# Optimization experiments

Measured on AMD Instinct MI355X. Metric: run time of the kernel, lower is better.

## Reference

```python
import jax, jax.numpy as jnp
import numpy as np

N = 50000      # nodes
E = 800000     # edges (before self-loops)
IN_DIM = 128
HID = 32
HEADS = 8
OUT_DIM = 16
NEG_SLOPE = 0.2  # PyG GATConv default


def setup_inputs() -> dict:
    key = jax.random.key(0)
    ks = jax.random.split(key, 12)
    x = jax.random.normal(ks[0], (N, IN_DIM), dtype=jnp.float32)
    edge_index = jax.random.randint(ks[1], (2, E), 0, N, dtype=jnp.int32)
    s = 0.1
    # layer 1: GATConv(IN_DIM -> HID, heads=HEADS, concat=True)
    W1 = jax.random.normal(ks[2], (IN_DIM, HEADS * HID), dtype=jnp.float32) * s
    a_src1 = jax.random.normal(ks[3], (HEADS, HID), dtype=jnp.float32) * s
    a_dst1 = jax.random.normal(ks[4], (HEADS, HID), dtype=jnp.float32) * s
    b1 = jax.random.normal(ks[5], (HEADS * HID,), dtype=jnp.float32) * s
    # layer 2: GATConv(HEADS*HID -> HID, heads=1, concat=True)
    W2 = jax.random.normal(ks[6], (HEADS * HID, HID), dtype=jnp.float32) * s
    a_src2 = jax.random.normal(ks[7], (1, HID), dtype=jnp.float32) * s
    a_dst2 = jax.random.normal(ks[8], (1, HID), dtype=jnp.float32) * s
    b2 = jax.random.normal(ks[9], (HID,), dtype=jnp.float32) * s
    # output Linear(HID -> OUT_DIM)
    Wout = jax.random.normal(ks[10], (HID, OUT_DIM), dtype=jnp.float32) * s
    bout = jax.random.normal(ks[11], (OUT_DIM,), dtype=jnp.float32) * s
    return {"x": x, "edge_index": edge_index, "W1": W1, "a_src1": a_src1,
            "a_dst1": a_dst1, "b1": b1, "W2": W2, "a_src2": a_src2,
            "a_dst2": a_dst2, "b2": b2, "Wout": Wout, "bout": bout}


def _gat_conv(x, src, dst, W, a_src, a_dst, b, num_nodes):
    """PyG GATConv (eval mode): linear proj, edge attention logits,
    segment-softmax over incoming edges per dst node, weighted scatter-sum.
    src/dst already include self-loops. Returns [N, H, D]."""
    H, D = a_src.shape
    h = (x @ W).reshape(num_nodes, H, D)                 # [N,H,D]
    alpha_s = jnp.einsum('nhd,hd->nh', h, a_src)         # [N,H]
    alpha_d = jnp.einsum('nhd,hd->nh', h, a_dst)         # [N,H]
    e = jax.nn.leaky_relu(alpha_s[src] + alpha_d[dst], NEG_SLOPE)  # [Etot,H]
    # numerically-stable segment softmax over edges grouped by dst
    m = jax.ops.segment_max(e, dst, num_segments=num_nodes)        # [N,H]
    ex = jnp.exp(e - m[dst])
    den = jax.ops.segment_sum(ex, dst, num_segments=num_nodes)     # [N,H]
    alpha = ex / (den[dst] + 1e-16)                                 # [Etot,H]
    out = jax.ops.segment_sum(alpha[:, :, None] * h[src], dst,
                              num_segments=num_nodes)               # [N,H,D]
    return out, b


def reference(x, edge_index, W1, a_src1, a_dst1, b1, W2, a_src2, a_dst2, b2,
              Wout, bout):
    n = x.shape[0]
    loop = jnp.arange(n, dtype=edge_index.dtype)
    src = jnp.concatenate([edge_index[0], loop])  # PyG add_self_loops=True
    dst = jnp.concatenate([edge_index[1], loop])
    o1, _ = _gat_conv(x, src, dst, W1, a_src1, a_dst1, b1, n)
    h1 = jax.nn.elu(o1.reshape(n, -1) + b1)       # concat heads -> [N, H*D]
    o2, _ = _gat_conv(h1, src, dst, W2, a_src2, a_dst2, b2, n)
    h2 = jax.nn.elu(o2.reshape(n, -1) + b2)       # heads=1 -> [N, HID]
    return h2 @ Wout + bout                        # [N, OUT_DIM]
```

## Files before the change

### kernel.cpp

```cpp
#include <hip/hip_runtime.h>
#include <math.h>

#define IN_DIM 128
#define HID 32
#define HEADS 8
#define OUT_DIM 16
#define NEG_SLOPE 0.2f


__global__ void count_kernel(const int* __restrict__ ei, int* __restrict__ counts,
                             int E, int N) {
    int e = blockIdx.x * 256 + threadIdx.x;
    int Etot = E + N;
    if (e >= Etot) return;
    int dst = (e < E) ? ei[E + e] : (e - E);
    atomicAdd(&counts[dst], 1);
}

__global__ __launch_bounds__(1024) void scan_kernel(const int* __restrict__ counts,
                                                    int* __restrict__ off,
                                                    int* __restrict__ pos, int N) {
    __shared__ int wsum[16];
    __shared__ int wbase[16];
    __shared__ int running_s;
    int tid = threadIdx.x;
    int lane = tid & 63, wid = tid >> 6;
    if (tid == 0) running_s = 0;
    __syncthreads();
    const int CH = 4096;
    int nchunk = (N + CH - 1) / CH;
    for (int c = 0; c < nchunk; ++c) {
        int base_i = c * CH + tid * 4;
        int v0 = (base_i + 0 < N) ? counts[base_i + 0] : 0;
        int v1 = (base_i + 1 < N) ? counts[base_i + 1] : 0;
        int v2 = (base_i + 2 < N) ? counts[base_i + 2] : 0;
        int v3 = (base_i + 3 < N) ? counts[base_i + 3] : 0;
        int tsum = v0 + v1 + v2 + v3;
        int x = tsum;
        #pragma unroll
        for (int ofs = 1; ofs < 64; ofs <<= 1) {
            int y = __shfl_up(x, ofs, 64);
            if (lane >= ofs) x += y;
        }
        if (lane == 63) wsum[wid] = x;
        __syncthreads();
        if (wid == 0) {
            int w = (lane < 16) ? wsum[lane] : 0;
            #pragma unroll
            for (int ofs = 1; ofs < 64; ofs <<= 1) {
                int y = __shfl_up(w, ofs, 64);
                if (lane >= ofs) w += y;
            }
            if (lane < 16) wbase[lane] = w;
        }
        __syncthreads();
        int chunk_base = running_s;
        int wave_excl = (wid == 0) ? 0 : wbase[wid - 1];
        int thr_excl = x - tsum;
        int b = chunk_base + wave_excl + thr_excl;
        if (base_i + 0 < N) { off[base_i + 0] = b; pos[base_i + 0] = b; } b += v0;
        if (base_i + 1 < N) { off[base_i + 1] = b; pos[base_i + 1] = b; } b += v1;
        if (base_i + 2 < N) { off[base_i + 2] = b; pos[base_i + 2] = b; } b += v2;
        if (base_i + 3 < N) { off[base_i + 3] = b; pos[base_i + 3] = b; }
        __syncthreads();
        if (tid == 0) running_s = chunk_base + wbase[15];
        __syncthreads();
    }
    if (tid == 0) off[N] = running_s;
}

__global__ void fill_kernel(const int* __restrict__ ei, int* __restrict__ pos,
                            int* __restrict__ csr_src, int E, int N) {
    int e = blockIdx.x * 256 + threadIdx.x;
    int Etot = E + N;
    if (e >= Etot) return;
    int src, dst;
    if (e < E) { src = ei[e]; dst = ei[E + e]; }
    else       { src = e - E; dst = e - E; }
    int idx = atomicAdd(&pos[dst], 1);
    csr_src[idx] = src;
}

__global__ __launch_bounds__(256) void gemm1_kernel(const float* __restrict__ x,
                                                    const float* __restrict__ W,
                                                    float* __restrict__ hp, int N) {
    __shared__ float4 xs4[32 * 32];
    int n0 = blockIdx.x * 32;
    int t = threadIdx.x;
    int rows = min(32, N - n0);
    const float4* xg = (const float4*)(x + (size_t)n0 * IN_DIM);
    int nf4 = rows * 32;
    for (int idx = t; idx < 1024; idx += 256)
        xs4[idx] = (idx < nf4) ? xg[idx] : make_float4(0.f, 0.f, 0.f, 0.f);
    __syncthreads();

    int c4 = t & 63;
    int r0 = (t >> 6) * 8;
    const float4* W4 = (const float4*)W;
    float4 acc[8];
    #pragma unroll
    for (int i = 0; i < 8; ++i) acc[i] = make_float4(0.f, 0.f, 0.f, 0.f);

    #pragma unroll 4
    for (int k4 = 0; k4 < 32; ++k4) {
        float4 w0 = W4[(k4 * 4 + 0) * 64 + c4];
        float4 w1 = W4[(k4 * 4 + 1) * 64 + c4];
        float4 w2 = W4[(k4 * 4 + 2) * 64 + c4];
        float4 w3 = W4[(k4 * 4 + 3) * 64 + c4];
        #pragma unroll
        for (int i = 0; i < 8; ++i) {
            float4 xq = xs4[(r0 + i) * 32 + k4];
            acc[i].x += xq.x * w0.x + xq.y * w1.x + xq.z * w2.x + xq.w * w3.x;
            acc[i].y += xq.x * w0.y + xq.y * w1.y + xq.z * w2.y + xq.w * w3.y;
            acc[i].z += xq.x * w0.z + xq.y * w1.z + xq.z * w2.z + xq.w * w3.z;
            acc[i].w += xq.x * w0.w + xq.y * w1.w + xq.z * w2.w + xq.w * w3.w;
        }
    }
    float4* hp4 = (float4*)hp;
    #pragma unroll
    for (int i = 0; i < 8; ++i)
        if (r0 + i < rows)
            hp4[(size_t)(n0 + r0 + i) * 64 + c4] = acc[i];
}

__global__ void alpha1_kernel(const float* __restrict__ hp,
                              const float* __restrict__ a_src,
                              const float* __restrict__ a_dst,
                              float* __restrict__ as, float* __restrict__ ad, int NH) {
    int t = blockIdx.x * 256 + threadIdx.x;
    if (t >= NH) return;
    int h = t & 7;
    const float4* hv  = (const float4*)(hp + (size_t)t * 32);
    const float4* av  = (const float4*)(a_src + h * 32);
    const float4* bv  = (const float4*)(a_dst + h * 32);
    float ss = 0.f, sd = 0.f;
    #pragma unroll
    for (int k = 0; k < 8; ++k) {
        float4 xv = hv[k], a = av[k], b = bv[k];
        ss += xv.x * a.x + xv.y * a.y + xv.z * a.z + xv.w * a.w;
        sd += xv.x * b.x + xv.y * b.y + xv.z * b.z + xv.w * b.w;
    }
    as[t] = ss;
    ad[t] = sd;
}

__global__ __launch_bounds__(256) void attn1_kernel(const int* __restrict__ off,
                                                    const int* __restrict__ csr_src,
                                                    const float* __restrict__ as,
                                                    const float* __restrict__ ad,
                                                    const float* __restrict__ hp,
                                                    const float* __restrict__ bias,
                                                    float* __restrict__ out, int N) {
    __shared__ float sred[4][8];
    __shared__ float ws[32][8];
    __shared__ int   ss[32];
    __shared__ float sinv[8];
    int n = blockIdx.x;
    int t = threadIdx.x;
    int wid = t >> 6, lane = t & 63;
    int beg = off[n], end = off[n + 1];
    int h8 = t & 7;
    int ie = t >> 3;
    float adn = ad[n * 8 + h8];

    float m = -INFINITY;
    for (int i = beg + ie; i < end; i += 32) {
        float e = as[csr_src[i] * 8 + h8] + adn;
        e = (e > 0.f) ? e : NEG_SLOPE * e;
        m = fmaxf(m, e);
    }
    m = fmaxf(m, __shfl_xor(m, 8, 64));
    m = fmaxf(m, __shfl_xor(m, 16, 64));
    m = fmaxf(m, __shfl_xor(m, 32, 64));
    if (lane < 8) sred[wid][lane] = m;
    __syncthreads();
    m = fmaxf(fmaxf(sred[0][h8], sred[1][h8]), fmaxf(sred[2][h8], sred[3][h8]));
    __syncthreads();

    int hh = t >> 5;
    float den_part = 0.f;
    float acc = 0.f;
    const float* hpt = hp + t;
    for (int c0 = beg; c0 < end; c0 += 32) {
        int i = c0 + ie;
        float w = 0.f; int s = 0;
        if (i < end) {
            s = csr_src[i];
            float e = as[s * 8 + h8] + adn;
            e = (e > 0.f) ? e : NEG_SLOPE * e;
            w = expf(e - m);
        }
        den_part += w;
        __syncthreads();
        ws[ie][h8] = w;
        if (h8 == 0) ss[ie] = s;
        __syncthreads();
        int cnt = min(32, end - c0);
        for (int j = 0; j < cnt; ++j) {
            int sj = __builtin_amdgcn_readfirstlane(ss[j]);
            acc += ws[j][hh] * hpt[(size_t)sj * 256];
        }
    }
    den_part += __shfl_xor(den_part, 8, 64);
    den_part += __shfl_xor(den_part, 16, 64);
    den_part += __shfl_xor(den_part, 32, 64);
    if (lane < 8) sred[wid][lane] = den_part;
    __syncthreads();
    if (t < 8) {
        float den = sred[0][t] + sred[1][t] + sred[2][t] + sred[3][t];
        sinv[t] = 1.f / (den + 1e-16f);
    }
    __syncthreads();
    float v = acc * sinv[hh] + bias[t];
    out[(size_t)n * 256 + t] = (v > 0.f) ? v : expm1f(v);
}

__global__ __launch_bounds__(256) void gemm2_kernel(const float* __restrict__ h1,
                                                    const float* __restrict__ W2,
                                                    float* __restrict__ hp2, int N) {
    __shared__ float hs[8 * 256];
    int n0 = blockIdx.x * 8;
    int t = threadIdx.x;
    int rows = min(8, N - n0);
    const float4* hg = (const float4*)(h1 + (size_t)n0 * 256);
    float4* hs4 = (float4*)hs;
    int nf4 = rows * 64;
    for (int idx = t; idx < 512; idx += 256)
        hs4[idx] = (idx < nf4) ? hg[idx] : make_float4(0.f, 0.f, 0.f, 0.f);
    __syncthreads();
    int i = t >> 5, j = t & 31;
    const float4* hrow = (const float4*)(hs + i * 256);
    float acc = 0.f;
    for (int k4 = 0; k4 < 64; ++k4) {
        float4 hv = hrow[k4];
        int k = k4 * 4;
        acc += hv.x * W2[(k + 0) * 32 + j] + hv.y * W2[(k + 1) * 32 + j]
             + hv.z * W2[(k + 2) * 32 + j] + hv.w * W2[(k + 3) * 32 + j];
    }
    if (i < rows) hp2[(size_t)(n0 + i) * 32 + j] = acc;
}

__global__ void alpha2_kernel(const float* __restrict__ hp2,
                              const float* __restrict__ a_src,
                              const float* __restrict__ a_dst,
                              float* __restrict__ as, float* __restrict__ ad, int N) {
    int t = blockIdx.x * 256 + threadIdx.x;
    if (t >= N) return;
    const float4* hv = (const float4*)(hp2 + (size_t)t * 32);
    const float4* av = (const float4*)a_src;
    const float4* bv = (const float4*)a_dst;
    float ss = 0.f, sd = 0.f;
    #pragma unroll
    for (int k = 0; k < 8; ++k) {
        float4 xv = hv[k], a = av[k], b = bv[k];
        ss += xv.x * a.x + xv.y * a.y + xv.z * a.z + xv.w * a.w;
        sd += xv.x * b.x + xv.y * b.y + xv.z * b.z + xv.w * b.w;
    }
    as[t] = ss;
    ad[t] = sd;
}

__global__ __launch_bounds__(256) void attn2_kernel(const int* __restrict__ off,
                                                    const int* __restrict__ csr_src,
                                                    const float* __restrict__ as,
                                                    const float* __restrict__ ad,
                                                    const float* __restrict__ hp2,
                                                    const float* __restrict__ b2,
                                                    float* __restrict__ h2, int N) {
    int g = threadIdx.x >> 5, d = threadIdx.x & 31;
    int n = blockIdx.x * 8 + g;
    if (n >= N) return;
    int beg = off[n], end = off[n + 1];
    float adn = ad[n];

    float m = -INFINITY;
    for (int i = beg + d; i < end; i += 32) {
        float e = as[csr_src[i]] + adn;
        e = (e > 0.f) ? e : NEG_SLOPE * e;
        m = fmaxf(m, e);
    }
    #pragma unroll
    for (int mask = 16; mask >= 1; mask >>= 1) m = fmaxf(m, __shfl_xor(m, mask, 32));

    float den_part = 0.f;
    float acc = 0.f;
    for (int c0 = beg; c0 < end; c0 += 32) {
        int i = c0 + d;
        float w = 0.f; int s = 0;
        if (i < end) {
            s = csr_src[i];
            float e = as[s] + adn;
            e = (e > 0.f) ? e : NEG_SLOPE * e;
            w = expf(e - m);
        }
        den_part += w;
        int cnt = min(32, end - c0);
        for (int j = 0; j < cnt; ++j) {
            float wj = __shfl(w, j, 32);
            int   sj = __shfl(s, j, 32);
            acc += wj * hp2[(size_t)sj * 32 + d];
        }
    }
    #pragma unroll
    for (int mask = 16; mask >= 1; mask >>= 1) den_part += __shfl_xor(den_part, mask, 32);
    float inv = 1.f / (den_part + 1e-16f);

    float v = acc * inv + b2[d];
    h2[(size_t)n * 32 + d] = (v > 0.f) ? v : expm1f(v);
}

__global__ void out_kernel(const float* __restrict__ h2,
                           const float* __restrict__ Wout,
                           const float* __restrict__ bout,
                           float* __restrict__ out, int N) {
    int t = blockIdx.x * 256 + threadIdx.x;
    if (t >= N * OUT_DIM) return;
    int n = t >> 4, j = t & 15;
    const float* hr = h2 + (size_t)n * 32;
    float acc = bout[j];
    #pragma unroll
    for (int k = 0; k < 32; ++k)
        acc += hr[k] * Wout[k * OUT_DIM + j];
    out[t] = acc;
}


extern "C" void kernel_launch(void* const* d_in, const int* in_sizes, int n_in,
                              void* d_out, int out_size, void* d_ws, size_t ws_size,
                              hipStream_t stream) {
    const float* x      = (const float*)d_in[0];
    const int*   ei     = (const int*)d_in[1];
    const float* W1     = (const float*)d_in[2];
    const float* a_src1 = (const float*)d_in[3];
    const float* a_dst1 = (const float*)d_in[4];
    const float* b1     = (const float*)d_in[5];
    const float* W2     = (const float*)d_in[6];
    const float* a_src2 = (const float*)d_in[7];
    const float* a_dst2 = (const float*)d_in[8];
    const float* b2     = (const float*)d_in[9];
    const float* Wout   = (const float*)d_in[10];
    const float* bout   = (const float*)d_in[11];
    float* out = (float*)d_out;

    const int N = in_sizes[0] / IN_DIM;
    const int E = in_sizes[1] / 2;
    const int Etot = E + N;

    char* p = (char*)d_ws;
    auto alloc = [&](size_t bytes) -> void* {
        void* r = (void*)p;
        p += (bytes + 255) & ~(size_t)255;
        return r;
    };
    float* hp1    = (float*)alloc((size_t)N * 256 * 4);
    float* h1     = (float*)alloc((size_t)N * 256 * 4);
    float* as1    = (float*)alloc((size_t)N * 8 * 4);
    float* ad1    = (float*)alloc((size_t)N * 8 * 4);
    float* hp2    = (float*)alloc((size_t)N * 32 * 4);
    float* as2    = (float*)alloc((size_t)N * 4);
    float* ad2    = (float*)alloc((size_t)N * 4);
    float* h2     = (float*)alloc((size_t)N * 32 * 4);
    int*   counts = (int*)alloc((size_t)N * 4);
    int*   off    = (int*)alloc((size_t)(N + 1) * 4);
    int*   pos    = (int*)alloc((size_t)N * 4);
    int*   csr    = (int*)alloc((size_t)Etot * 4);
    (void)ws_size;

    hipMemsetAsync(counts, 0, (size_t)N * 4, stream);
    int eb = (Etot + 255) / 256;
    count_kernel<<<eb, 256, 0, stream>>>(ei, counts, E, N);
    scan_kernel<<<1, 1024, 0, stream>>>(counts, off, pos, N);
    fill_kernel<<<eb, 256, 0, stream>>>(ei, pos, csr, E, N);

    gemm1_kernel<<<(N + 31) / 32, 256, 0, stream>>>(x, W1, hp1, N);
    alpha1_kernel<<<(N * 8 + 255) / 256, 256, 0, stream>>>(hp1, a_src1, a_dst1, as1, ad1, N * 8);
    attn1_kernel<<<N, 256, 0, stream>>>(off, csr, as1, ad1, hp1, b1, h1, N);

    gemm2_kernel<<<(N + 7) / 8, 256, 0, stream>>>(h1, W2, hp2, N);
    alpha2_kernel<<<(N + 255) / 256, 256, 0, stream>>>(hp2, a_src2, a_dst2, as2, ad2, N);
    attn2_kernel<<<(N + 7) / 8, 256, 0, stream>>>(off, csr, as2, ad2, hp2, b2, h2, N);

    out_kernel<<<(N * OUT_DIM + 255) / 256, 256, 0, stream>>>(h2, Wout, bout, out, N);
}
```

Before: 616.1 us.

## Fuse attention-logit dot products into GEMMs and output linear into attn2

Computes the per-node, per-head source and destination attention logits inside gemm1 and gemm2 using wave shuffles, so the separate alpha kernels and their re-read of the projected features go away. The final output linear layer is folded into attn2, which removes the h2 intermediate buffer and one launch. attn1's inner loop also drops the readfirstlane on the source index. That scalarization loss could hurt the hottest loop.

```diff
diff --git a/kernel.cpp b/kernel.cpp
--- a/kernel.cpp
+++ b/kernel.cpp
@@ -83,7 +83,11 @@
 
 __global__ __launch_bounds__(256) void gemm1_kernel(const float* __restrict__ x,
                                                     const float* __restrict__ W,
-                                                    float* __restrict__ hp, int N) {
+                                                    const float* __restrict__ a_src,
+                                                    const float* __restrict__ a_dst,
+                                                    float* __restrict__ hp,
+                                                    float* __restrict__ as,
+                                                    float* __restrict__ ad, int N) {
     __shared__ float4 xs4[32 * 32];
     int n0 = blockIdx.x * 32;
     int t = threadIdx.x;
@@ -121,27 +125,22 @@
     for (int i = 0; i < 8; ++i)
         if (r0 + i < rows)
             hp4[(size_t)(n0 + r0 + i) * 64 + c4] = acc[i];
-}
-
-__global__ void alpha1_kernel(const float* __restrict__ hp,
-                              const float* __restrict__ a_src,
-                              const float* __restrict__ a_dst,
-                              float* __restrict__ as, float* __restrict__ ad, int NH) {
-    int t = blockIdx.x * 256 + threadIdx.x;
-    if (t >= NH) return;
-    int h = t & 7;
-    const float4* hv  = (const float4*)(hp + (size_t)t * 32);
-    const float4* av  = (const float4*)(a_src + h * 32);
-    const float4* bv  = (const float4*)(a_dst + h * 32);
-    float ss = 0.f, sd = 0.f;
-    #pragma unroll
-    for (int k = 0; k < 8; ++k) {
-        float4 xv = hv[k], a = av[k], b = bv[k];
-        ss += xv.x * a.x + xv.y * a.y + xv.z * a.z + xv.w * a.w;
-        sd += xv.x * b.x + xv.y * b.y + xv.z * b.z + xv.w * b.w;
-    }
-    as[t] = ss;
-    ad[t] = sd;
+
+    int h = c4 >> 3, q = c4 & 7;
+    float4 av = ((const float4*)a_src)[h * 8 + q];
+    float4 bv = ((const float4*)a_dst)[h * 8 + q];
+    #pragma unroll
+    for (int i = 0; i < 8; ++i) {
+        float ps = acc[i].x * av.x + acc[i].y * av.y + acc[i].z * av.z + acc[i].w * av.w;
+        float pd = acc[i].x * bv.x + acc[i].y * bv.y + acc[i].z * bv.z + acc[i].w * bv.w;
+        ps += __shfl_xor(ps, 1, 64); pd += __shfl_xor(pd, 1, 64);
+        ps += __shfl_xor(ps, 2, 64); pd += __shfl_xor(pd, 2, 64);
+        ps += __shfl_xor(ps, 4, 64); pd += __shfl_xor(pd, 4, 64);
+        if (q == 0 && r0 + i < rows) {
+            as[(size_t)(n0 + r0 + i) * 8 + h] = ps;
+            ad[(size_t)(n0 + r0 + i) * 8 + h] = pd;
+        }
+    }
 }
 
 __global__ __launch_bounds__(256) void attn1_kernel(const int* __restrict__ off,
@@ -180,7 +179,6 @@
     int hh = t >> 5;
     float den_part = 0.f;
     float acc = 0.f;
-    const float* hpt = hp + t;
     for (int c0 = beg; c0 < end; c0 += 32) {
         int i = c0 + ie;
         float w = 0.f; int s = 0;
@@ -196,10 +194,8 @@
         if (h8 == 0) ss[ie] = s;
         __syncthreads();
         int cnt = min(32, end - c0);
-        for (int j = 0; j < cnt; ++j) {
-            int sj = __builtin_amdgcn_readfirstlane(ss[j]);
-            acc += ws[j][hh] * hpt[(size_t)sj * 256];
-        }
+        for (int j = 0; j < cnt; ++j)
+            acc += ws[j][hh] * hp[(size_t)ss[j] * 256 + t];
     }
     den_part += __shfl_xor(den_part, 8, 64);
     den_part += __shfl_xor(den_part, 16, 64);
@@ -217,7 +213,11 @@
 
 __global__ __launch_bounds__(256) void gemm2_kernel(const float* __restrict__ h1,
                                                     const float* __restrict__ W2,
-                                                    float* __restrict__ hp2, int N) {
+                                                    const float* __restrict__ a_src,
+                                                    const float* __restrict__ a_dst,
+                                                    float* __restrict__ hp2,
+                                                    float* __restrict__ as,
+                                                    float* __restrict__ ad, int N) {
     __shared__ float hs[8 * 256];
     int n0 = blockIdx.x * 8;
     int t = threadIdx.x;
@@ -238,26 +238,18 @@
              + hv.z * W2[(k + 2) * 32 + j] + hv.w * W2[(k + 3) * 32 + j];
     }
     if (i < rows) hp2[(size_t)(n0 + i) * 32 + j] = acc;
-}
-
-__global__ void alpha2_kernel(const float* __restrict__ hp2,
-                              const float* __restrict__ a_src,
-                              const float* __restrict__ a_dst,
-                              float* __restrict__ as, float* __restrict__ ad, int N) {
-    int t = blockIdx.x * 256 + threadIdx.x;
-    if (t >= N) return;
-    const float4* hv = (const float4*)(hp2 + (size_t)t * 32);
-    const float4* av = (const float4*)a_src;
-    const float4* bv = (const float4*)a_dst;
-    float ss = 0.f, sd = 0.f;
-    #pragma unroll
-    for (int k = 0; k < 8; ++k) {
-        float4 xv = hv[k], a = av[k], b = bv[k];
-        ss += xv.x * a.x + xv.y * a.y + xv.z * a.z + xv.w * a.w;
-        sd += xv.x * b.x + xv.y * b.y + xv.z * b.z + xv.w * b.w;
-    }
-    as[t] = ss;
-    ad[t] = sd;
+
+    float ps = acc * a_src[j];
+    float pd = acc * a_dst[j];
+    #pragma unroll
+    for (int mask = 16; mask >= 1; mask >>= 1) {
+        ps += __shfl_xor(ps, mask, 32);
+        pd += __shfl_xor(pd, mask, 32);
+    }
+    if (j == 0 && i < rows) {
+        as[n0 + i] = ps;
+        ad[n0 + i] = pd;
+    }
 }
 
 __global__ __launch_bounds__(256) void attn2_kernel(const int* __restrict__ off,
@@ -266,7 +258,9 @@
                                                     const float* __restrict__ ad,
                                                     const float* __restrict__ hp2,
                                                     const float* __restrict__ b2,
-                                                    float* __restrict__ h2, int N) {
+                                                    const float* __restrict__ Wout,
+                                                    const float* __restrict__ bout,
+                                                    float* __restrict__ out, int N) {
     int g = threadIdx.x >> 5, d = threadIdx.x & 31;
     int n = blockIdx.x * 8 + g;
     if (n >= N) return;
@@ -306,22 +300,16 @@
     float inv = 1.f / (den_part + 1e-16f);
 
     float v = acc * inv + b2[d];
-    h2[(size_t)n * 32 + d] = (v > 0.f) ? v : expm1f(v);
-}
-
-__global__ void out_kernel(const float* __restrict__ h2,
-                           const float* __restrict__ Wout,
-                           const float* __restrict__ bout,
-                           float* __restrict__ out, int N) {
-    int t = blockIdx.x * 256 + threadIdx.x;
-    if (t >= N * OUT_DIM) return;
-    int n = t >> 4, j = t & 15;
-    const float* hr = h2 + (size_t)n * 32;
-    float acc = bout[j];
-    #pragma unroll
-    for (int k = 0; k < 32; ++k)
-        acc += hr[k] * Wout[k * OUT_DIM + j];
-    out[t] = acc;
+    float h2d = (v > 0.f) ? v : expm1f(v);
+
+    float o = 0.f;
+    #pragma unroll
+    for (int k = 0; k < 32; ++k) {
+        float hk = __shfl(h2d, k, 32);
+        if (d < 16) o += hk * Wout[k * OUT_DIM + d];
+    }
+    if (d < 16)
+        out[(size_t)n * OUT_DIM + d] = o + bout[d];
 }
 
 
@@ -359,7 +347,6 @@
     float* hp2    = (float*)alloc((size_t)N * 32 * 4);
     float* as2    = (float*)alloc((size_t)N * 4);
     float* ad2    = (float*)alloc((size_t)N * 4);
-    float* h2     = (float*)alloc((size_t)N * 32 * 4);
     int*   counts = (int*)alloc((size_t)N * 4);
     int*   off    = (int*)alloc((size_t)(N + 1) * 4);
     int*   pos    = (int*)alloc((size_t)N * 4);
@@ -372,13 +359,9 @@
     scan_kernel<<<1, 1024, 0, stream>>>(counts, off, pos, N);
     fill_kernel<<<eb, 256, 0, stream>>>(ei, pos, csr, E, N);
 
-    gemm1_kernel<<<(N + 31) / 32, 256, 0, stream>>>(x, W1, hp1, N);
-    alpha1_kernel<<<(N * 8 + 255) / 256, 256, 0, stream>>>(hp1, a_src1, a_dst1, as1, ad1, N * 8);
+    gemm1_kernel<<<(N + 31) / 32, 256, 0, stream>>>(x, W1, a_src1, a_dst1, hp1, as1, ad1, N);
     attn1_kernel<<<N, 256, 0, stream>>>(off, csr, as1, ad1, hp1, b1, h1, N);
 
-    gemm2_kernel<<<(N + 7) / 8, 256, 0, stream>>>(h1, W2, hp2, N);
-    alpha2_kernel<<<(N + 255) / 256, 256, 0, stream>>>(hp2, a_src2, a_dst2, as2, ad2, N);
-    attn2_kernel<<<(N + 7) / 8, 256, 0, stream>>>(off, csr, as2, ad2, hp2, b2, h2, N);
-
-    out_kernel<<<(N * OUT_DIM + 255) / 256, 256, 0, stream>>>(h2, Wout, bout, out, N);
-}
+    gemm2_kernel<<<(N + 7) / 8, 256, 0, stream>>>(h1, W2, a_src2, a_dst2, hp2, as2, ad2, N);
+    attn2_kernel<<<(N + 7) / 8, 256, 0, stream>>>(off, csr, as2, ad2, hp2, b2, Wout, bout, out, N);
+}
```

After: 527.3 us. 14.4% less time.
